# Kernel tuning notes

Measured on AMD Instinct MI355X. Metric: run time of the kernel, lower is better.

## Reference

```python
import jax, jax.numpy as jnp
import numpy as np

USER_NUM = 1000
SKILL_NUM = 256
K_HIDDEN = 128
N_ITEMS = 4096
SEQ_LEN = 8192

def setup_inputs() -> dict:
    key = jax.random.key(0)
    k1, k2, k3 = jax.random.split(key, 3)
    # binary Q-matrix: item -> skill incidence (p=0.1 sparsity)
    Q_matrix = (jax.random.uniform(k1, (N_ITEMS, SKILL_NUM)) < 0.1).astype(jnp.float32)
    items = jax.random.randint(k2, (SEQ_LEN,), 0, N_ITEMS)
    skill_embedding = jax.random.normal(k3, (USER_NUM, SKILL_NUM, K_HIDDEN), dtype=jnp.float32) * 0.01
    user = 3
    return {"user": user, "Q_matrix": Q_matrix, "items": items, "skill_embedding": skill_embedding}

def reference(user, Q_matrix, items, skill_embedding):
    # Original double loop: ret[pos] = sum over skills where Q[item, s] == 1 of E[user, s]
    # == Q_matrix[items] @ skill_embedding[user]  (Q entries are 0/1)
    q_rows = Q_matrix[items]                 # [L, S] gather
    emb = skill_embedding[user]              # [S, K]
    return jnp.einsum('ls,sk->lk', q_rows, emb)  # [L, K]
```

## Files before the change

### kernel.cpp

```cpp
#include <hip/hip_runtime.h>


#define SKILL_NUM 256
#define K_HIDDEN  128

__global__ __launch_bounds__(256) void item_emb_kernel(
    const int*   __restrict__ user_p,
    const float* __restrict__ Q,
    const int*   __restrict__ items,
    const float* __restrict__ E_all,
    float*       __restrict__ out,
    int L)
{
    const int wave = threadIdx.x >> 6;
    const int lane = threadIdx.x & 63;
    const int l    = blockIdx.x * 4 + wave;
    if (l >= L) return;

    const int item = items[l];
    const float* __restrict__ qrow = Q + (size_t)item * SKILL_NUM;
    const float2* __restrict__ E2 = (const float2*)(
        E_all + (size_t)user_p[0] * (SKILL_NUM * K_HIDDEN));

    const float q0 = qrow[lane];
    const float q1 = qrow[64 + lane];
    const float q2 = qrow[128 + lane];
    const float q3 = qrow[192 + lane];
    unsigned long long m0 = __ballot(q0 != 0.0f);
    unsigned long long m1 = __ballot(q1 != 0.0f);
    unsigned long long m2 = __ballot(q2 != 0.0f);
    unsigned long long m3 = __ballot(q3 != 0.0f);

    float ax = 0.0f, ay = 0.0f;

    auto scan = [&](unsigned long long mask, int base) {
        while (mask) {
            const int s0 = base + __builtin_ctzll(mask);
            mask &= mask - 1;
            if (mask) {
                const int s1 = base + __builtin_ctzll(mask);
                mask &= mask - 1;
                const float2 a = E2[(size_t)s0 * 64 + lane];
                const float2 b = E2[(size_t)s1 * 64 + lane];
                ax += a.x + b.x;
                ay += a.y + b.y;
            } else {
                const float2 a = E2[(size_t)s0 * 64 + lane];
                ax += a.x;
                ay += a.y;
            }
        }
    };
    scan(m0, 0);
    scan(m1, 64);
    scan(m2, 128);
    scan(m3, 192);

    float2 r;
    r.x = ax;
    r.y = ay;
    ((float2*)out)[(size_t)l * 64 + lane] = r;
}

extern "C" void kernel_launch(void* const* d_in, const int* in_sizes, int n_in,
                              void* d_out, int out_size, void* d_ws, size_t ws_size,
                              hipStream_t stream) {
    const int*   user_p = (const int*)  d_in[0];
    const float* Q      = (const float*)d_in[1];
    const int*   items  = (const int*)  d_in[2];
    const float* E_all  = (const float*)d_in[3];
    float*       out    = (float*)      d_out;

    const int L = in_sizes[2];
    const int blocks = (L + 3) / 4;

    item_emb_kernel<<<blocks, 256, 0, stream>>>(user_p, Q, items, E_all, out, L);
}
```

Measured before the change: 172.9 us.

## Compact nonzero skill indices in LDS and batch eight embedding loads per iteration

Each wave now loads its Q row as one float4 per lane, ballots the nonzero entries, and writes the matching skill indices in compacted order into shared memory. It then walks the list eight at a time, issuing eight independent embedding row loads before accumulating into two partial sums. This is meant to raise memory-level parallelism compared with the serial ctz loop, which had at most two loads in flight. It adds a block-wide barrier and LDS traffic, and reads stale slots on the final partial group, which are loaded but discarded. Reading stale slots is safe because indices are bytes below 256.

```diff
diff --git a/kernel.cpp b/kernel.cpp
--- a/kernel.cpp
+++ b/kernel.cpp
@@ -12,54 +12,79 @@
     float*       __restrict__ out,
     int L)
 {
+    __shared__ __align__(8) unsigned char sidx[4][SKILL_NUM];
+
     const int wave = threadIdx.x >> 6;
     const int lane = threadIdx.x & 63;
     const int l    = blockIdx.x * 4 + wave;
-    if (l >= L) return;
+    const bool valid = (l < L);
 
-    const int item = items[l];
-    const float* __restrict__ qrow = Q + (size_t)item * SKILL_NUM;
     const float2* __restrict__ E2 = (const float2*)(
         E_all + (size_t)user_p[0] * (SKILL_NUM * K_HIDDEN));
 
-    const float q0 = qrow[lane];
-    const float q1 = qrow[64 + lane];
-    const float q2 = qrow[128 + lane];
-    const float q3 = qrow[192 + lane];
-    unsigned long long m0 = __ballot(q0 != 0.0f);
-    unsigned long long m1 = __ballot(q1 != 0.0f);
-    unsigned long long m2 = __ballot(q2 != 0.0f);
-    unsigned long long m3 = __ballot(q3 != 0.0f);
+    int n = 0;
+    if (valid) {
+        const int item = items[l];
+        const float4 qv = ((const float4*)(Q + (size_t)item * SKILL_NUM))[lane];
+        const unsigned long long m0 = __ballot(qv.x != 0.0f);
+        const unsigned long long m1 = __ballot(qv.y != 0.0f);
+        const unsigned long long m2 = __ballot(qv.z != 0.0f);
+        const unsigned long long m3 = __ballot(qv.w != 0.0f);
+        const int c0 = __popcll(m0), c1 = __popcll(m1), c2 = __popcll(m2);
+        const unsigned long long below = (1ull << lane) - 1ull;
+        n = c0 + c1 + c2 + __popcll(m3);
+        if (qv.x != 0.0f) sidx[wave][           __popcll(m0 & below)] = (unsigned char)(4*lane+0);
+        if (qv.y != 0.0f) sidx[wave][c0       + __popcll(m1 & below)] = (unsigned char)(4*lane+1);
+        if (qv.z != 0.0f) sidx[wave][c0+c1    + __popcll(m2 & below)] = (unsigned char)(4*lane+2);
+        if (qv.w != 0.0f) sidx[wave][c0+c1+c2 + __popcll(m3 & below)] = (unsigned char)(4*lane+3);
+    }
+    __syncthreads();
+    if (!valid) return;
 
-    float ax = 0.0f, ay = 0.0f;
+    float ax0 = 0.f, ay0 = 0.f, ax1 = 0.f, ay1 = 0.f;
 
-    auto scan = [&](unsigned long long mask, int base) {
-        while (mask) {
-            const int s0 = base + __builtin_ctzll(mask);
-            mask &= mask - 1;
-            if (mask) {
-                const int s1 = base + __builtin_ctzll(mask);
-                mask &= mask - 1;
-                const float2 a = E2[(size_t)s0 * 64 + lane];
-                const float2 b = E2[(size_t)s1 * 64 + lane];
-                ax += a.x + b.x;
-                ay += a.y + b.y;
-            } else {
-                const float2 a = E2[(size_t)s0 * 64 + lane];
-                ax += a.x;
-                ay += a.y;
-            }
+    const unsigned long long* packp = (const unsigned long long*)&sidx[wave][0];
+    const int nb = (n + 7) >> 3;
+    for (int b = 0; b < nb; ++b) {
+        const unsigned long long pack = packp[b];
+        const int s0 = __builtin_amdgcn_readfirstlane((int)( pack        & 0xff));
+        const int s1 = __builtin_amdgcn_readfirstlane((int)((pack >>  8) & 0xff));
+        const int s2 = __builtin_amdgcn_readfirstlane((int)((pack >> 16) & 0xff));
+        const int s3 = __builtin_amdgcn_readfirstlane((int)((pack >> 24) & 0xff));
+        const int s4 = __builtin_amdgcn_readfirstlane((int)((pack >> 32) & 0xff));
+        const int s5 = __builtin_amdgcn_readfirstlane((int)((pack >> 40) & 0xff));
+        const int s6 = __builtin_amdgcn_readfirstlane((int)((pack >> 48) & 0xff));
+        const int s7 = __builtin_amdgcn_readfirstlane((int)((pack >> 56) & 0xff));
+        const float2 a0 = E2[(size_t)(s0 * 64) + lane];
+        const float2 a1 = E2[(size_t)(s1 * 64) + lane];
+        const float2 a2 = E2[(size_t)(s2 * 64) + lane];
+        const float2 a3 = E2[(size_t)(s3 * 64) + lane];
+        const float2 a4 = E2[(size_t)(s4 * 64) + lane];
+        const float2 a5 = E2[(size_t)(s5 * 64) + lane];
+        const float2 a6 = E2[(size_t)(s6 * 64) + lane];
+        const float2 a7 = E2[(size_t)(s7 * 64) + lane];
+        const int base = b << 3;
+        if (base + 8 <= n) {
+            ax0 += a0.x + a1.x;  ay0 += a0.y + a1.y;
+            ax1 += a2.x + a3.x;  ay1 += a2.y + a3.y;
+            ax0 += a4.x + a5.x;  ay0 += a4.y + a5.y;
+            ax1 += a6.x + a7.x;  ay1 += a6.y + a7.y;
+        } else {
+            const int r = n - base;
+            if (r > 0) { ax0 += a0.x; ay0 += a0.y; }
+            if (r > 1) { ax0 += a1.x; ay0 += a1.y; }
+            if (r > 2) { ax1 += a2.x; ay1 += a2.y; }
+            if (r > 3) { ax1 += a3.x; ay1 += a3.y; }
+            if (r > 4) { ax0 += a4.x; ay0 += a4.y; }
+            if (r > 5) { ax0 += a5.x; ay0 += a5.y; }
+            if (r > 6) { ax1 += a6.x; ay1 += a6.y; }
         }
-    };
-    scan(m0, 0);
-    scan(m1, 64);
-    scan(m2, 128);
-    scan(m3, 192);
+    }
 
-    float2 r;
-    r.x = ax;
-    r.y = ay;
-    ((float2*)out)[(size_t)l * 64 + lane] = r;
+    float2 rr;
+    rr.x = ax0 + ax1;
+    rr.y = ay0 + ay1;
+    ((float2*)out)[(size_t)l * 64 + lane] = rr;
 }
 
 extern "C" void kernel_launch(void* const* d_in, const int* in_sizes, int n_in,
```

Result: no change. 174.0 us (+0.6%).
